# Optimization experiments

Measured on AMD Instinct MI355X. Metric: run time of the kernel, lower is better.

The kernel has to match this reference:

```python
import jax, jax.numpy as jnp
import numpy as np

C = 512
GROUPS = 32
EPS = 1e-6


def setup_inputs() -> dict:
    key = jax.random.key(0)
    ks = jax.random.split(key, 10)
    s = 0.02
    return {
        "x": jax.random.normal(ks[0], (2, C, 64, 64), dtype=jnp.float32),
        "gn_scale": jnp.ones((C,), jnp.float32),
        "gn_bias": jnp.zeros((C,), jnp.float32),
        "wq": jax.random.normal(ks[1], (C, C), jnp.float32) * s,
        "bq": jnp.zeros((C,), jnp.float32),
        "wk": jax.random.normal(ks[2], (C, C), jnp.float32) * s,
        "bk": jnp.zeros((C,), jnp.float32),
        "wv": jax.random.normal(ks[3], (C, C), jnp.float32) * s,
        "bv": jnp.zeros((C,), jnp.float32),
        "wo": jax.random.normal(ks[4], (C, C), jnp.float32) * s,
        "bo": jnp.zeros((C,), jnp.float32),
    }


def group_norm(x, scale, bias):
    # x: [b, c, h, w]; 32 groups over channel dim
    b, c, h, w = x.shape
    xg = x.reshape(b, GROUPS, c // GROUPS, h, w)
    mean = jnp.mean(xg, axis=(2, 3, 4), keepdims=True)
    var = jnp.var(xg, axis=(2, 3, 4), keepdims=True)
    xg = (xg - mean) * jax.lax.rsqrt(var + EPS)
    x = xg.reshape(b, c, h, w)
    return x * scale[None, :, None, None] + bias[None, :, None, None]


def reference(x, gn_scale, gn_bias, wq, bq, wk, bk, wv, bv, wo, bo):
    b, c, h, w = x.shape
    n = h * w
    hn = group_norm(x, gn_scale, gn_bias).reshape(b, c, n)  # [b,c,n]
    # 1x1 conv == channel matmul: out[b,o,n] = W[o,i] @ h[b,i,n] + bias
    q = jnp.einsum('oi,bin->bon', wq, hn) + bq[None, :, None]
    k = jnp.einsum('oi,bin->bon', wk, hn) + bk[None, :, None]
    v = jnp.einsum('oi,bin->bon', wv, hn) + bv[None, :, None]
    # weight[b, i, j] = q_i . k_j, softmax over j
    scale = int(c) ** (-0.5)
    weight = jnp.einsum('bci,bcj->bij', q, k) * scale  # [b,n,n]
    weight = jax.nn.softmax(weight, axis=2)
    # h[b,c,i] = sum_j v[b,c,j] * weight[b,i,j]
    out = jnp.einsum('bcj,bij->bci', v, weight)
    out = jnp.einsum('oi,bin->bon', wo, out) + bo[None, :, None]
    return out.reshape(b, c, h, w) + x
```

## Files before the change

kernel.cpp:

```cpp
#include <hip/hip_runtime.h>
#include <hip/hip_bf16.h>


typedef __attribute__((ext_vector_type(8))) short short8_t;
typedef __attribute__((ext_vector_type(4))) short short4_t;
typedef __attribute__((ext_vector_type(4))) float f32x4;

__device__ __forceinline__ void gload16(const void* g, void* l) {
  __builtin_amdgcn_global_load_lds(
      (const __attribute__((address_space(1))) void*)g,
      (__attribute__((address_space(3))) void*)l, 16, 0, 0);
}

__device__ __forceinline__ short f2bf_bits(float f) {
  __hip_bfloat16 h = __float2bfloat16(f);
  return *reinterpret_cast<short*>(&h);
}
__device__ __forceinline__ float bfbits2f(short s) {
  union { unsigned int u; float f; } c;
  c.u = ((unsigned int)(unsigned short)s) << 16;
  return c.f;
}

__global__ __launch_bounds__(512)
void s_gemm8(const __hip_bfloat16* __restrict__ qk,
             __hip_bfloat16* __restrict__ P, float* __restrict__ part2,
             float c)
{
  const long long QKz = 4096LL * 1024;
  const long long SS  = 4096LL * 4096;

  const int b = blockIdx.x;
  const int bz = b >> 8;
  const int r = b & 255, xcd = r & 7, sl = r >> 3;
  const int bm = (xcd >> 1) * 4 + (sl & 3);
  const int bn = (xcd & 1) * 8 + (sl >> 2);

  const __hip_bfloat16* Aq = qk + (size_t)bz * QKz;
  const __hip_bfloat16* Bk = Aq + 512;

  const int tid = threadIdx.x;
  const int wid = tid >> 6, l = tid & 63;
  const int wrM = wid >> 2, wcN = wid & 3;
  const int lhi = l >> 4, llo = l & 15;

  __shared__ char sm[2 * 65536];

  f32x4 acc[2][2][4][2] = {};
  short8_t af[4][2], bf[2][2];

  const int rIn = l >> 3;
  const int colSw = 8 * ((l & 7) ^ (rIn & 7));
  const __hip_bfloat16* gA = Aq + (size_t)(bm * 256 + rIn) * 1024 + colSw;
  const __hip_bfloat16* gB = Bk + (size_t)(bn * 256 + rIn) * 1024 + colSw;

  auto STG = [&](int mat, int half, int t) {
    const __hip_bfloat16* src = mat ? gB : gA;
    char* dst = sm + (t & 1) * 65536 + mat * 32768;
    const int rb = half * 128 + wid * 16;
    gload16(src + (size_t)rb * 1024 + t * 64, dst + rb * 128);
    gload16(src + (size_t)(rb + 8) * 1024 + t * 64, dst + (rb + 8) * 128);
  };

#define GSTART(N) do {                                                        \
    asm volatile("s_waitcnt vmcnt(" #N ")" ::: "memory");                     \
    __builtin_amdgcn_sched_barrier(0);                                        \
    __builtin_amdgcn_s_barrier();                                             \
    __builtin_amdgcn_sched_barrier(0);                                        \
  } while (0)

#define PHASE(MH, NH, RBUF, LA, LB, ...) do {                                 \
    const char* bbA = sm + (RBUF) * 65536;                                    \
    const char* bbB = bbA + 32768;                                            \
    if (LA) {                                                                 \
      _Pragma("unroll") for (int m = 0; m < 4; ++m) {                         \
        const int rowA = (MH) * 128 + wrM * 64 + m * 16 + llo;                \
        _Pragma("unroll") for (int kk = 0; kk < 2; ++kk)                      \
          af[m][kk] = *(const short8_t*)(bbA + rowA * 128 +                   \
                        (((kk * 4 + lhi) ^ (rowA & 7)) * 16));                \
      }                                                                       \
    }                                                                         \
    if (LB) {                                                                 \
      _Pragma("unroll") for (int n = 0; n < 2; ++n) {                         \
        const int rowB = (NH) * 128 + wcN * 32 + n * 16 + llo;                \
        _Pragma("unroll") for (int kk = 0; kk < 2; ++kk)                      \
          bf[n][kk] = *(const short8_t*)(bbB + rowB * 128 +                   \
                        (((kk * 4 + lhi) ^ (rowB & 7)) * 16));                \
      }                                                                       \
    }                                                                         \
    __VA_ARGS__;                                                              \
    __builtin_amdgcn_sched_barrier(0);                                        \
    __builtin_amdgcn_s_barrier();                                             \
    __builtin_amdgcn_sched_barrier(0);                                        \
    __builtin_amdgcn_s_setprio(1);                                            \
    _Pragma("unroll") for (int kk = 0; kk < 2; ++kk)                          \
      _Pragma("unroll") for (int m = 0; m < 4; ++m)                           \
        _Pragma("unroll") for (int n = 0; n < 2; ++n)                         \
          acc[MH][NH][m][n] = __builtin_amdgcn_mfma_f32_16x16x32_bf16(        \
              af[m][kk], bf[n][kk], acc[MH][NH][m][n], 0, 0, 0);              \
    __builtin_amdgcn_s_setprio(0);                                            \
    __builtin_amdgcn_sched_barrier(0);                                        \
    __builtin_amdgcn_s_barrier();                                             \
    __builtin_amdgcn_sched_barrier(0);                                        \
  } while (0)

  STG(0, 0, 0); STG(1, 0, 0); STG(0, 1, 0); STG(1, 1, 0);
  STG(0, 0, 1); STG(1, 0, 1); STG(0, 1, 1); STG(1, 1, 1);
  asm volatile("s_waitcnt vmcnt(0)" ::: "memory");
  __builtin_amdgcn_sched_barrier(0);
  __builtin_amdgcn_s_barrier();
  __builtin_amdgcn_sched_barrier(0);

  for (int i = 0; i < 3; ++i) {
    const int t1 = 2 * i + 1, t2 = 2 * i + 2, t3 = 2 * i + 3;
    GSTART(6);
    PHASE(0, 0, 0, 1, 1, if (i >= 1) STG(1, 0, t1));
    PHASE(0, 1, 0, 0, 1, STG(0, 0, t2));
    PHASE(1, 1, 0, 1, 0, STG(1, 1, t2));
    PHASE(1, 0, 0, 0, 1, STG(0, 1, t2));
    GSTART(6);
    PHASE(0, 0, 1, 1, 1, STG(1, 0, t2));
    PHASE(0, 1, 1, 0, 1, STG(0, 0, t3));
    PHASE(1, 1, 1, 1, 0, STG(1, 1, t3));
    PHASE(1, 0, 1, 0, 1, STG(0, 1, t3));
  }
  {
    GSTART(6);
    PHASE(0, 0, 0, 1, 1, STG(1, 0, 7));
    PHASE(0, 1, 0, 0, 1, );
    PHASE(1, 1, 0, 1, 0, );
    PHASE(1, 0, 0, 0, 1, );
    GSTART(0);
    PHASE(0, 0, 1, 1, 1, );
    PHASE(0, 1, 1, 0, 1, );
    PHASE(1, 1, 1, 1, 0, );
    PHASE(1, 0, 1, 0, 1, );
  }
#undef PHASE
#undef GSTART

  __hip_bfloat16* Pb = P + (size_t)bz * SS;
  float rp[2][4][4];
#pragma unroll
  for (int Mh = 0; Mh < 2; ++Mh)
#pragma unroll
    for (int m = 0; m < 4; ++m)
#pragma unroll
      for (int rr = 0; rr < 4; ++rr) {
        const int grow = bm * 256 + Mh * 128 + wrM * 64 + m * 16 + lhi * 4 + rr;
        float s = 0.f;
#pragma unroll
        for (int Nh = 0; Nh < 2; ++Nh)
#pragma unroll
          for (int n = 0; n < 2; ++n) {
            const int gcol = bn * 256 + Nh * 128 + wcN * 32 + n * 16 + llo;
            const float v = exp2f(acc[Mh][Nh][m][n][rr] * c);
            Pb[(size_t)grow * 4096 + gcol] = __float2bfloat16(v);
            s += v;
          }
        rp[Mh][m][rr] = s;
      }
#pragma unroll
  for (int Mh = 0; Mh < 2; ++Mh)
#pragma unroll
    for (int m = 0; m < 4; ++m)
#pragma unroll
      for (int rr = 0; rr < 4; ++rr) {
        float s = rp[Mh][m][rr];
        s += __shfl_xor(s, 1); s += __shfl_xor(s, 2);
        s += __shfl_xor(s, 4); s += __shfl_xor(s, 8);
        rp[Mh][m][rr] = s;
      }
  __syncthreads();
  float* rsl = (float*)sm;
  if (llo == 0) {
#pragma unroll
    for (int Mh = 0; Mh < 2; ++Mh)
#pragma unroll
      for (int m = 0; m < 4; ++m)
#pragma unroll
        for (int rr = 0; rr < 4; ++rr) {
          const int rl = Mh * 128 + wrM * 64 + m * 16 + lhi * 4 + rr;
          rsl[rl * 4 + wcN] = rp[Mh][m][rr];
        }
  }
  __syncthreads();
  if (tid < 256) {
    const float s = rsl[tid * 4] + rsl[tid * 4 + 1] + rsl[tid * 4 + 2] + rsl[tid * 4 + 3];
    part2[((size_t)bz * 16 + bn) * 4096 + bm * 256 + tid] = s;
  }
}

__global__ __launch_bounds__(256)
void rs_final(const float* __restrict__ part2, float* __restrict__ rs)
{
  const int i = blockIdx.x * 256 + threadIdx.x;
  const int z = i >> 12, row = i & 4095;
  float s = 0.f;
#pragma unroll
  for (int bn = 0; bn < 16; ++bn)
    s += part2[((size_t)z * 16 + bn) * 4096 + row];
  rs[(size_t)z * 4096 + row] = 1.f / s;
}

template<int OUTF, int BIASMODE, int RESID, int PIPE, int SWZ, int MF, int NORM>
__global__ __launch_bounds__(256, 2)
void gemm_nt(const __hip_bfloat16* __restrict__ A,
             const __hip_bfloat16* __restrict__ B,
             void* __restrict__ Cv,
             const float* __restrict__ bias,
             const float* __restrict__ resid,
             const float* __restrict__ rnorm,
             float scale, int M, int N, int K,
             int lda, int ldb, int ldc,
             long long strA, long long strB, long long strC, long long strR)
{
  int bm, bn, bz;
  if (SWZ == 0) {
    bm = blockIdx.x; bn = blockIdx.y; bz = blockIdx.z;
  } else if (SWZ == 2) {
    const int b = blockIdx.x;
    bz = b >> 10;
    const int b2 = b & 1023;
    const int xcd = b2 & 7, s = b2 >> 3;
    bm = (xcd >> 1) * 8 + (s & 7);
    bn = (xcd & 1) * 16 + (s >> 3);
  } else {
    const int b = blockIdx.x;
    const int xcd = b & 7, slot = b >> 3;
    bm = slot & 7;
    const int panel = xcd * 8 + (slot >> 3);
    bn = panel & 31; bz = panel >> 5;
  }
  const int z = bz;
  A += (size_t)z * strA;
  B += (size_t)z * strB;

  const int tid = threadIdx.x;
  const int w = tid >> 6, l = tid & 63;
  const int wr = w >> 1, wc = w & 1;
  const int lhi = l >> 4, llo = l & 15;
  const int m0 = bm * (MF * 32), n0 = bn * 128;

  constexpr int BUFSZ = MF * 4096 + 16384;
  __shared__ char sm[(PIPE ? 2 : 1) * BUFSZ];

  f32x4 acc[MF][4] = {};

  const int rowInCh = l >> 3;
  const int colOff = 8 * ((l & 7) ^ (rowInCh & 7));

  const __hip_bfloat16* gAr[MF];
  const __hip_bfloat16* gBr[4];
#pragma unroll
  for (int j = 0; j < MF; ++j)
    gAr[j] = A + (size_t)(m0 + w * (8 * MF) + j * 8 + rowInCh) * lda + colOff;
#pragma unroll
  for (int r = 0; r < 4; ++r)
    gBr[r] = B + (size_t)(n0 + w * 32 + r * 8 + rowInCh) * ldb + colOff;

  auto stage = [&](int kt, int buf) {
    char* sA = sm + buf * BUFSZ;
    char* sB = sA + MF * 4096;
    const int ko = kt * 64;
#pragma unroll
    for (int j = 0; j < MF; ++j)
      gload16(gAr[j] + ko, sA + (w * MF + j) * 1024);
#pragma unroll
    for (int r = 0; r < 4; ++r)
      gload16(gBr[r] + ko, sB + (w * 4 + r) * 1024);
  };

  auto compute = [&](int buf) {
    char* sA = sm + buf * BUFSZ;
    char* sB = sA + MF * 4096;
#pragma unroll
    for (int kk = 0; kk < 2; ++kk) {
      short8_t af[MF], bfv[4];
#pragma unroll
      for (int m = 0; m < MF; ++m) {
        const int row = wr * (16 * MF) + m * 16 + llo;
        const int inner = ((kk * 4 + lhi) ^ (row & 7)) * 16;
        af[m] = *(const short8_t*)(sA + row * 128 + inner);
      }
#pragma unroll
      for (int n = 0; n < 4; ++n) {
        const int row = wc * 64 + n * 16 + llo;
        const int inner = ((kk * 4 + lhi) ^ (row & 7)) * 16;
        bfv[n] = *(const short8_t*)(sB + row * 128 + inner);
      }
#pragma unroll
      for (int m = 0; m < MF; ++m)
#pragma unroll
        for (int n = 0; n < 4; ++n)
          acc[m][n] = __builtin_amdgcn_mfma_f32_16x16x32_bf16(af[m], bfv[n], acc[m][n], 0, 0, 0);
    }
  };

  const int nkt = K >> 6;
  if (PIPE) {
    stage(0, 0);
    __syncthreads();
    int cur = 0;
    for (int kt = 0; kt < nkt; ++kt) {
      if (kt + 1 < nkt) stage(kt + 1, cur ^ 1);
      compute(cur);
      __syncthreads();
      cur ^= 1;
    }
  } else {
    for (int kt = 0; kt < nkt; ++kt) {
      __syncthreads();
      stage(kt, 0);
      __syncthreads();
      compute(0);
    }
  }

#pragma unroll
  for (int m = 0; m < MF; ++m) {
#pragma unroll
    for (int r = 0; r < 4; ++r) {
      const int grow = m0 + wr * (16 * MF) + m * 16 + lhi * 4 + r;
#pragma unroll
      for (int n = 0; n < 4; ++n) {
        const int gcol = n0 + wc * 64 + n * 16 + llo;
        float v = acc[m][n][r] * scale;
        if (NORM) v *= rnorm[(size_t)z * 4096 + gcol];
        if (BIASMODE == 1) v += bias[grow];
        if (BIASMODE == 2) v += bias[gcol];
        const size_t idx = (size_t)z * strC + (size_t)grow * ldc + gcol;
        if (RESID) v += resid[(size_t)z * strR + (size_t)grow * ldc + gcol];
        if (OUTF == 0) ((__hip_bfloat16*)Cv)[idx] = __float2bfloat16(v);
        else           ((float*)Cv)[idx] = v;
      }
    }
  }
}

__global__ __launch_bounds__(256)
void gn_partial(const float* __restrict__ x, float* __restrict__ part)
{
  const int g = blockIdx.x, sl = blockIdx.y, z = blockIdx.z;
  const int tid = threadIdx.x;
  const float* xf = x + (size_t)z * 512 * 4096 + (size_t)g * 16 * 4096 + (size_t)sl * 4096;
  const float4* px = reinterpret_cast<const float4*>(xf);
  float s = 0.f, q = 0.f;
#pragma unroll
  for (int i = 0; i < 4; ++i) {
    float4 v = px[tid + i * 256];
    s += v.x + v.y + v.z + v.w;
    q += v.x * v.x + v.y * v.y + v.z * v.z + v.w * v.w;
  }
#pragma unroll
  for (int o = 32; o; o >>= 1) { s += __shfl_xor(s, o); q += __shfl_xor(q, o); }
  __shared__ float rs[4], rq[4];
  if ((tid & 63) == 0) { rs[tid >> 6] = s; rq[tid >> 6] = q; }
  __syncthreads();
  if (tid == 0) {
    s = rs[0] + rs[1] + rs[2] + rs[3];
    q = rq[0] + rq[1] + rq[2] + rq[3];
    part[(((size_t)z * 32 + g) * 16 + sl) * 2 + 0] = s;
    part[(((size_t)z * 32 + g) * 16 + sl) * 2 + 1] = q;
  }
}

__global__ __launch_bounds__(64)
void gn_finalize(const float* __restrict__ part, float* __restrict__ stats, int n)
{
  const int i = threadIdx.x;
  if (i >= n) return;
  float s = 0.f, q = 0.f;
#pragma unroll
  for (int sl = 0; sl < 16; ++sl) {
    s += part[(i * 16 + sl) * 2 + 0];
    q += part[(i * 16 + sl) * 2 + 1];
  }
  const float mean = s * (1.0f / 65536.0f);
  const float var = q * (1.0f / 65536.0f) - mean * mean;
  stats[i * 2 + 0] = mean;
  stats[i * 2 + 1] = rsqrtf(var + 1e-6f);
}

__global__ __launch_bounds__(256)
void gn_apply_t(const float* __restrict__ x, const float* __restrict__ stats,
                const float* __restrict__ gns, const float* __restrict__ gnb,
                __hip_bfloat16* __restrict__ ht)
{
  const int st = blockIdx.x, ct = blockIdx.y, z = blockIdx.z;
  const int tid = threadIdx.x;
  __shared__ float tile[64][65];
  const float* xb = x + (size_t)z * 512 * 4096;
  const int lane64 = tid & 63, rr = tid >> 6;
#pragma unroll
  for (int pp = 0; pp < 16; ++pp) {
    const int cl = pp * 4 + rr;
    const int c = ct * 64 + cl;
    const int g = c >> 4;
    const float mean = stats[(z * 32 + g) * 2 + 0];
    const float rstd = stats[(z * 32 + g) * 2 + 1];
    const float val = xb[(size_t)c * 4096 + st * 64 + lane64];
    tile[cl][lane64] = (val - mean) * rstd * gns[c] + gnb[c];
  }
  __syncthreads();
  __hip_bfloat16* hb = ht + (size_t)z * 4096 * 512;
#pragma unroll
  for (int pp = 0; pp < 16; ++pp) {
    const int sl = pp * 4 + rr;
    const int s = st * 64 + sl;
    hb[(size_t)s * 512 + ct * 64 + lane64] = __float2bfloat16(tile[lane64][sl]);
  }
}

__global__ __launch_bounds__(256)
void softmax_rows(__hip_bfloat16* __restrict__ S, long long strZ)
{
  const int row = blockIdx.x, z = blockIdx.y;
  __hip_bfloat16* p = S + (size_t)z * strZ + (size_t)row * 4096;
  const int tid = threadIdx.x;
  short8_t a = *(const short8_t*)(p + tid * 16);
  short8_t b = *(const short8_t*)(p + tid * 16 + 8);
  float v[16];
#pragma unroll
  for (int i = 0; i < 8; ++i) { v[i] = bfbits2f(a[i]); v[8 + i] = bfbits2f(b[i]); }
  float m = v[0];
#pragma unroll
  for (int i = 1; i < 16; ++i) m = fmaxf(m, v[i]);
#pragma unroll
  for (int o = 32; o; o >>= 1) m = fmaxf(m, __shfl_xor(m, o));
  __shared__ float red[8];
  if ((tid & 63) == 0) red[tid >> 6] = m;
  __syncthreads();
  m = fmaxf(fmaxf(red[0], red[1]), fmaxf(red[2], red[3]));
  float s = 0.f;
#pragma unroll
  for (int i = 0; i < 16; ++i) { v[i] = exp2f((v[i] - m) * 1.44269504f); s += v[i]; }
#pragma unroll
  for (int o = 32; o; o >>= 1) s += __shfl_xor(s, o);
  __syncthreads();
  if ((tid & 63) == 0) red[4 + (tid >> 6)] = s;
  __syncthreads();
  s = red[4] + red[5] + red[6] + red[7];
  const float inv = 1.f / s;
#pragma unroll
  for (int i = 0; i < 8; ++i) { a[i] = f2bf_bits(v[i] * inv); b[i] = f2bf_bits(v[8 + i] * inv); }
  *(short8_t*)(p + tid * 16) = a;
  *(short8_t*)(p + tid * 16 + 8) = b;
}

__global__ __launch_bounds__(256)
void cast3(const float* __restrict__ w0, const float* __restrict__ w1,
           const float* __restrict__ w2, __hip_bfloat16* __restrict__ out)
{
  const int j = blockIdx.y;
  const float* src = (j == 0) ? w0 : (j == 1) ? w1 : w2;
  const int i = blockIdx.x * 256 + threadIdx.x;
  float4 v = reinterpret_cast<const float4*>(src)[i];
  short4_t o;
  o[0] = f2bf_bits(v.x); o[1] = f2bf_bits(v.y);
  o[2] = f2bf_bits(v.z); o[3] = f2bf_bits(v.w);
  *reinterpret_cast<short4_t*>((short*)out + (size_t)j * 262144 + (size_t)i * 4) = o;
}

__global__ __launch_bounds__(256)
void transpose_cast(const float* __restrict__ w, __hip_bfloat16* __restrict__ wt)
{
  __shared__ float tile[64][65];
  const int ct = blockIdx.x, it = blockIdx.y;
  const int tid = threadIdx.x;
  const int lane = tid & 63, rr = tid >> 6;
#pragma unroll
  for (int p = 0; p < 16; ++p) {
    const int cl = p * 4 + rr;
    tile[cl][lane] = w[(size_t)(ct * 64 + cl) * 512 + it * 64 + lane];
  }
  __syncthreads();
#pragma unroll
  for (int p = 0; p < 16; ++p) {
    const int il = p * 4 + rr;
    wt[(size_t)(it * 64 + il) * 512 + ct * 64 + lane] = __float2bfloat16(tile[lane][il]);
  }
}

__global__ __launch_bounds__(64)
void prep_bias(const float* __restrict__ wo, const float* __restrict__ bv,
               const float* __restrict__ bo, const float* __restrict__ bq,
               const float* __restrict__ bk,
               float* __restrict__ bvo, float* __restrict__ bqk)
{
  const int o = blockIdx.x * 64 + threadIdx.x;
  const float4* row = reinterpret_cast<const float4*>(wo + (size_t)o * 512);
  const float4* b4 = reinterpret_cast<const float4*>(bv);
  float s = 0.f;
#pragma unroll 8
  for (int i = 0; i < 128; ++i) {
    float4 a = row[i], b = b4[i];
    s += a.x * b.x + a.y * b.y + a.z * b.z + a.w * b.w;
  }
  bvo[o] = s + bo[o];
  bqk[o] = bq[o];
  bqk[512 + o] = bk[o];
}

extern "C" void kernel_launch(void* const* d_in, const int* in_sizes, int n_in,
                              void* d_out, int out_size, void* d_ws, size_t ws_size,
                              hipStream_t stream)
{
  const float* x   = (const float*)d_in[0];
  const float* gns = (const float*)d_in[1];
  const float* gnb = (const float*)d_in[2];
  const float* wq  = (const float*)d_in[3];
  const float* bq  = (const float*)d_in[4];
  const float* wk  = (const float*)d_in[5];
  const float* bk  = (const float*)d_in[6];
  const float* wv  = (const float*)d_in[7];
  const float* bv  = (const float*)d_in[8];
  const float* wo  = (const float*)d_in[9];
  const float* bo  = (const float*)d_in[10];
  float* out = (float*)d_out;

  const int WB = 512 * 512;
  const long long HT  = 4096LL * 512;
  const long long QKz = 4096LL * 1024;
  const long long VOz = 512LL * 4096;
  const long long SS  = 4096LL * 4096;
  const long long CHW = 512LL * 4096;

  char* base = (char*)d_ws;
  size_t off = 0;
  auto alloc = [&](size_t b) { void* r = base + off; off = (off + b + 255) & ~(size_t)255; return r; };

  __hip_bfloat16* wbf = (__hip_bfloat16*)alloc((size_t)5 * WB * 2);
  float* bqk   = (float*)alloc(1024 * 4);
  float* bvo   = (float*)alloc(512 * 4);
  float* part  = (float*)alloc(2 * 32 * 16 * 2 * 4);
  float* stats = (float*)alloc(2 * 32 * 2 * 4);
  float* rsum  = (float*)alloc(2 * 4096 * 4);
  float* part2 = (float*)alloc((size_t)2 * 16 * 4096 * 4);
  const size_t fixed = off;

  const size_t qkB = (size_t)2 * QKz * 2;
  const size_t voB = (size_t)2 * VOz * 2;
  const size_t sB2 = (size_t)2 * SS * 2;
  const size_t sB1 = (size_t)SS * 2;
  const int MODE = (ws_size >= fixed + qkB + voB + sB2) ? 2 : 1;

  __hip_bfloat16* qk   = (__hip_bfloat16*)alloc(qkB);
  __hip_bfloat16* vo   = (__hip_bfloat16*)alloc(voB);
  const size_t sbufB = (MODE == 2) ? sB2 : sB1;
  __hip_bfloat16* sbuf = (__hip_bfloat16*)alloc(sbufB);
  __hip_bfloat16* ht = (__hip_bfloat16*)((char*)sbuf + sbufB - (size_t)2 * HT * 2);

  __hip_bfloat16* wqk = wbf;
  __hip_bfloat16* woB = wbf + 2 * WB;
  __hip_bfloat16* wvT = wbf + 3 * WB;
  __hip_bfloat16* wvo = wbf + 4 * WB;

  const float SC = 0.04419417382415922f;
  const float CEXP = SC * 1.4426950408889634f;

  cast3<<<dim3(256, 3), 256, 0, stream>>>(wq, wk, wo, wbf);
  transpose_cast<<<dim3(8, 8), 256, 0, stream>>>(wv, wvT);
  prep_bias<<<8, 64, 0, stream>>>(wo, bv, bo, bq, bk, bvo, bqk);
  gn_partial<<<dim3(32, 16, 2), 256, 0, stream>>>(x, part);
  gn_finalize<<<1, 64, 0, stream>>>(part, stats, 64);

  gemm_nt<0, 0, 0, 1, 0, 4, 0><<<dim3(4, 4, 1), 256, 0, stream>>>(
      woB, wvT, wvo, nullptr, nullptr, nullptr, 1.f, 512, 512, 512,
      512, 512, 512, 0, 0, 0, 0);

  gn_apply_t<<<dim3(64, 8, 2), 256, 0, stream>>>(x, stats, gns, gnb, ht);

  gemm_nt<0, 2, 0, 1, 0, 4, 0><<<dim3(32, 8, 2), 256, 0, stream>>>(
      ht, wqk, qk, bqk, nullptr, nullptr, 1.f, 4096, 1024, 512,
      512, 512, 1024, HT, 0, QKz, 0);

  gemm_nt<0, 0, 0, 1, 3, 2, 0><<<dim3(512, 1, 1), 256, 0, stream>>>(
      wvo, ht, vo, nullptr, nullptr, nullptr, 1.f, 512, 4096, 512,
      512, 512, 4096, 0, HT, VOz, 0);

  if (MODE == 2) {
    s_gemm8<<<512, 512, 0, stream>>>(qk, sbuf, part2, CEXP);
    rs_final<<<32, 256, 0, stream>>>(part2, rsum);
    gemm_nt<1, 1, 1, 1, 3, 2, 1><<<dim3(512, 1, 1), 256, 0, stream>>>(
        vo, sbuf, out, bvo, x, rsum, 1.f, 512, 4096, 4096,
        4096, 4096, 4096, VOz, SS, CHW, CHW);
  } else {
    for (int z = 0; z < 2; ++z) {
      gemm_nt<0, 0, 0, 0, 0, 4, 0><<<dim3(32, 32, 1), 256, 0, stream>>>(
          qk + (size_t)z * QKz, qk + (size_t)z * QKz + 512, sbuf, nullptr, nullptr,
          nullptr, SC, 4096, 4096, 512, 1024, 1024, 4096, 0, 0, 0, 0);
      softmax_rows<<<dim3(4096, 1), 256, 0, stream>>>(sbuf, 0);
      gemm_nt<1, 1, 1, 1, 0, 2, 0><<<dim3(8, 32, 1), 256, 0, stream>>>(
          vo + (size_t)z * VOz, sbuf, out + (size_t)z * CHW, bvo, x + (size_t)z * CHW,
          nullptr, 1.f, 512, 4096, 4096, 4096, 4096, 4096, 0, 0, 0, 0);
    }
  }
}
```

Baseline: 156.0 us.

## Restructure QK^T GEMM main loop into rolled pipeline with fused waitcnt barriers

Replaces the unrolled eight-phase double-buffer schedule with a rolled loop over K-tiles where the buffer is selected at runtime. B-tile loads for the next stage are issued together early, and A-tile loads later. The separate GSTART wait+barrier is folded into the last phase's trailing barrier with vmcnt(4)/vmcnt(0). The aim is to cut the number of barriers and the redundant sched_barriers per tile, and to change how prefetch overlaps with MFMA. The risk is that dropping sched_barriers lets the compiler reorder LDS reads around s_barrier, and the vmcnt counts must match the reordered issue pattern.

Result: no change. 155.4 us (-0.4%).

```diff
diff --git a/kernel.cpp b/kernel.cpp
--- a/kernel.cpp
+++ b/kernel.cpp
@@ -62,15 +62,8 @@
     gload16(src + (size_t)(rb + 8) * 1024 + t * 64, dst + (rb + 8) * 128);
   };
 
-#define GSTART(N) do {                                                        \
-    asm volatile("s_waitcnt vmcnt(" #N ")" ::: "memory");                     \
-    __builtin_amdgcn_sched_barrier(0);                                        \
-    __builtin_amdgcn_s_barrier();                                             \
-    __builtin_amdgcn_sched_barrier(0);                                        \
-  } while (0)
-
-#define PHASE(MH, NH, RBUF, LA, LB, ...) do {                                 \
-    const char* bbA = sm + (RBUF) * 65536;                                    \
+#define PHASE(MH, NH, LA, LB, VM, ...) do {                                   \
+    const char* bbA = sm + bsel * 65536;                                      \
     const char* bbB = bbA + 32768;                                            \
     if (LA) {                                                                 \
       _Pragma("unroll") for (int m = 0; m < 4; ++m) {                         \
@@ -89,7 +82,6 @@
       }                                                                       \
     }                                                                         \
     __VA_ARGS__;                                                              \
-    __builtin_amdgcn_sched_barrier(0);                                        \
     __builtin_amdgcn_s_barrier();                                             \
     __builtin_amdgcn_sched_barrier(0);                                        \
     __builtin_amdgcn_s_setprio(1);                                            \
@@ -99,7 +91,8 @@
           acc[MH][NH][m][n] = __builtin_amdgcn_mfma_f32_16x16x32_bf16(        \
               af[m][kk], bf[n][kk], acc[MH][NH][m][n], 0, 0, 0);              \
     __builtin_amdgcn_s_setprio(0);                                            \
-    __builtin_amdgcn_sched_barrier(0);                                        \
+    if ((VM) == 1) asm volatile("s_waitcnt vmcnt(4)" ::: "memory");           \
+    if ((VM) == 2) asm volatile("s_waitcnt vmcnt(0)" ::: "memory");           \
     __builtin_amdgcn_s_barrier();                                             \
     __builtin_amdgcn_sched_barrier(0);                                        \
   } while (0)
@@ -107,37 +100,20 @@
   STG(0, 0, 0); STG(1, 0, 0); STG(0, 1, 0); STG(1, 1, 0);
   STG(0, 0, 1); STG(1, 0, 1); STG(0, 1, 1); STG(1, 1, 1);
   asm volatile("s_waitcnt vmcnt(0)" ::: "memory");
-  __builtin_amdgcn_sched_barrier(0);
   __builtin_amdgcn_s_barrier();
   __builtin_amdgcn_sched_barrier(0);
 
-  for (int i = 0; i < 3; ++i) {
-    const int t1 = 2 * i + 1, t2 = 2 * i + 2, t3 = 2 * i + 3;
-    GSTART(6);
-    PHASE(0, 0, 0, 1, 1, if (i >= 1) STG(1, 0, t1));
-    PHASE(0, 1, 0, 0, 1, STG(0, 0, t2));
-    PHASE(1, 1, 0, 1, 0, STG(1, 1, t2));
-    PHASE(1, 0, 0, 0, 1, STG(0, 1, t2));
-    GSTART(6);
-    PHASE(0, 0, 1, 1, 1, STG(1, 0, t2));
-    PHASE(0, 1, 1, 0, 1, STG(0, 0, t3));
-    PHASE(1, 1, 1, 1, 0, STG(1, 1, t3));
-    PHASE(1, 0, 1, 0, 1, STG(0, 1, t3));
-  }
-  {
-    GSTART(6);
-    PHASE(0, 0, 0, 1, 1, STG(1, 0, 7));
-    PHASE(0, 1, 0, 0, 1, );
-    PHASE(1, 1, 0, 1, 0, );
-    PHASE(1, 0, 0, 0, 1, );
-    GSTART(0);
-    PHASE(0, 0, 1, 1, 1, );
-    PHASE(0, 1, 1, 0, 1, );
-    PHASE(1, 1, 1, 1, 0, );
-    PHASE(1, 0, 1, 0, 1, );
+  for (int t = 0; t < 8; ++t) {
+    const int bsel = t & 1;
+    const int stB = (t >= 1 && t < 7);
+    const int stA = (t < 6);
+    const int vm = (t < 6) ? 1 : (t == 6) ? 2 : 0;
+    PHASE(0, 0, 1, 1, 0, if (stB) { STG(1, 0, t + 1); STG(1, 1, t + 1); });
+    PHASE(0, 1, 0, 1, 0, if (stA) STG(0, 0, t + 2););
+    PHASE(1, 1, 1, 0, 0, );
+    PHASE(1, 0, 0, 1, vm, if (stA) STG(0, 1, t + 2););
   }
 #undef PHASE
-#undef GSTART
 
   __hip_bfloat16* Pb = P + (size_t)bz * SS;
   float rp[2][4][4];
```
